# Optimization experiments

Hardware: AMD Instinct MI355X
Metric: run time of the kernel (lower is better)

## Reference

```python
import jax, jax.numpy as jnp
import numpy as np
import itertools
from jax import lax

B, DIM, RES = 32, 256, 8
KEY_DIM, NUM_HEADS, ATTN_RATIO = 16, 8, 4
NH_KD = KEY_DIM * NUM_HEADS          # 128
DH = ATTN_RATIO * KEY_DIM * NUM_HEADS  # 512
HQKV = DH + 2 * NH_KD                # 768
N = RES ** 3                         # 512


def _bias_idxs():
    pts = np.array(list(itertools.product(range(RES), repeat=3)))  # [N,3]
    off = np.abs(pts[:, None, :] - pts[None, :, :])                # [N,N,3]
    return jnp.asarray(off[..., 0] * RES * RES + off[..., 1] * RES + off[..., 2], dtype=jnp.int32)


def setup_inputs() -> dict:
    key = jax.random.key(0)
    ks = jax.random.split(key, 12)
    s = 0.05
    return {
        "x": jax.random.normal(ks[0], (B, DIM, RES, RES, RES), jnp.float32),
        "qkv_w": jax.random.normal(ks[1], (HQKV, DIM), jnp.float32) * s,
        "qkv_scale": jax.random.uniform(ks[2], (HQKV,), jnp.float32, 0.5, 1.5),
        "qkv_bias": jax.random.normal(ks[3], (HQKV,), jnp.float32) * s,
        "dw_w": jax.random.normal(ks[4], (NH_KD, 1, 3, 3, 3), jnp.float32) * s,
        "dw_scale": jax.random.uniform(ks[5], (NH_KD,), jnp.float32, 0.5, 1.5),
        "dw_bias": jax.random.normal(ks[6], (NH_KD,), jnp.float32) * s,
        "attn_biases": jax.random.normal(ks[7], (NUM_HEADS, N), jnp.float32) * s,
        "proj_w": jax.random.normal(ks[8], (DIM, DH), jnp.float32) * s,
        "proj_scale": jax.random.uniform(ks[9], (DIM,), jnp.float32, 0.5, 1.5),
        "proj_bias": jax.random.normal(ks[10], (DIM,), jnp.float32) * s,
        "bias_idxs": _bias_idxs(),
    }


def _cbn(x, w, scale, bias):
    # 1x1x1 Conv3d (pointwise, no bias) + folded BatchNorm (per-channel affine)
    y = jnp.einsum('bcdhw,oc->bodhw', x, w)
    return y * scale[None, :, None, None, None] + bias[None, :, None, None, None]


def reference(x, qkv_w, qkv_scale, qkv_bias, dw_w, dw_scale, dw_bias,
              attn_biases, proj_w, proj_scale, proj_bias, bias_idxs):
    Bx, _, D, H, W = x.shape
    n = D * H * W
    scale = KEY_DIM ** -0.5

    qkv = _cbn(x, qkv_w, qkv_scale, qkv_bias)  # [B, 768, D,H,W]
    q = qkv[:, :NH_KD]
    k = qkv[:, NH_KD:2 * NH_KD]
    v = qkv[:, 2 * NH_KD:]

    # depthwise 3x3x3 conv on q + folded BN
    q = lax.conv_general_dilated(q, dw_w, (1, 1, 1), [(1, 1)] * 3,
                                 dimension_numbers=('NCDHW', 'OIDHW', 'NCDHW'),
                                 feature_group_count=NH_KD)
    q = q * dw_scale[None, :, None, None, None] + dw_bias[None, :, None, None, None]

    q = q.reshape(Bx, NUM_HEADS, KEY_DIM, n)
    k = k.reshape(Bx, NUM_HEADS, KEY_DIM, n)
    v = v.reshape(Bx, NUM_HEADS, DH // NUM_HEADS, n)

    attn = jnp.einsum('bhcn,bhcm->bhnm', q, k) * scale
    attn = attn + attn_biases[:, bias_idxs]          # gathered rel-pos bias [h,N,N]
    attn = jax.nn.softmax(attn, axis=-1)

    out = jnp.einsum('bhdm,bhnm->bhdn', v, attn)     # v @ attn^T
    out = out.reshape(Bx, DH, D, H, W)
    out = jax.nn.relu(out)
    return _cbn(out, proj_w, proj_scale, proj_bias)
```

## Files before the change

kernel.cpp:

```cpp
#include <hip/hip_runtime.h>

typedef unsigned int u32;
typedef unsigned short u16;
typedef __attribute__((ext_vector_type(8))) short bf16x8;
typedef __attribute__((ext_vector_type(4))) float f32x4;

constexpr int BATCH = 32;
constexpr int DIM   = 256;
constexpr int NPTS  = 512;
constexpr int NH    = 8;
constexpr int KD    = 16;
constexpr int DHEAD = 64;
constexpr int NH_KD = 128;
constexpr int DH    = 512;

__device__ __forceinline__ float bflo(u32 u){ return __uint_as_float(u << 16); }
__device__ __forceinline__ float bfhi(u32 u){ return __uint_as_float(u & 0xffff0000u); }
__device__ __forceinline__ float bf2f(u16 u){ return __uint_as_float(((u32)u) << 16); }

__device__ __forceinline__ u32 pack2bf(float a, float b){
  u32 r;
  asm("v_cvt_pk_bf16_f32 %0, %1, %2" : "=v"(r) : "v"(a), "v"(b));
  return r;
}
__device__ __forceinline__ u16 f2bf(float f){ return (u16)pack2bf(f, f); }

union B8 { bf16x8 v; uint2 u2[2]; uint4 u4; };

typedef const __attribute__((address_space(1))) unsigned int gu32_t;
typedef __attribute__((address_space(3))) unsigned int su32_t;
__device__ __forceinline__ void gld16(const u16* src, u16* ldsDst){
  __builtin_amdgcn_global_load_lds((gu32_t*)src, (su32_t*)ldsDst, 16, 0, 0);
}

__device__ __forceinline__ void quadtr(float v[4], int lq){
  float t[4], y[4];
  #pragma unroll
  for (int r = 0; r < 4; r++) t[r] = __shfl_xor(v[r], 1, 64);
  #pragma unroll
  for (int r = 0; r < 4; r++) y[r] = ((r & 1) == (lq & 1)) ? v[r] : t[r ^ 1];
  #pragma unroll
  for (int r = 0; r < 4; r++) t[r] = __shfl_xor(y[r], 2, 64);
  #pragma unroll
  for (int r = 0; r < 4; r++) v[r] = ((r & 2) == (lq & 2)) ? y[r] : t[r ^ 2];
}

__global__ __launch_bounds__(256) void k_pre(
    const float* __restrict__ wq, const float* __restrict__ sq,
    const float* __restrict__ wp, const float* __restrict__ sp,
    u32* __restrict__ wqb, u32* __restrict__ pwb,
    const float* __restrict__ x, u16* __restrict__ xbt,
    const float* __restrict__ ab, const int* __restrict__ bidx,
    u32* __restrict__ biasb)
{
  __shared__ u16 T[64*68];
  const int blk = blockIdx.x;
  const int tid = threadIdx.x;

  if (blk < 640){
    int t = blk * 256 + tid;
    if (t < 98304){
      int i = 2*t;
      float s = sq[i >> 8];
      wqb[t] = pack2bf(wq[i]*s, wq[i+1]*s);
    } else {
      int j = t - 98304;
      int i = 2*j;
      float s = sp[i >> 9];
      pwb[j] = pack2bf(wp[i]*s, wp[i+1]*s);
    }
  } else if (blk < 1664){
    const int bk = blk - 640;
    const int b = bk >> 5, ct = (bk >> 3) & 3, nt = bk & 7;
    const int c0 = ct*64, n0 = nt*64;

    const float* xb = x + ((size_t)b*DIM + c0)*NPTS + n0;
    #pragma unroll
    for (int it = 0; it < 4; it++){
      int cc = (tid >> 4) + it*16;
      int nn = (tid & 15) * 4;
      float4 v = *(const float4*)(xb + (size_t)cc*NPTS + nn);
      u32* dst = (u32*)&T[cc*68 + nn];
      dst[0] = pack2bf(v.x, v.y);
      dst[1] = pack2bf(v.z, v.w);
    }
    __syncthreads();
    u16* ob = xbt + ((size_t)b*NPTS + n0)*DIM + c0;
    #pragma unroll
    for (int it = 0; it < 4; it++){
      int nn = (tid >> 4) + it*16;
      int cc = (tid & 15) * 4;
      uint2 w;
      w.x = (u32)T[(cc+0)*68 + nn] | ((u32)T[(cc+1)*68 + nn] << 16);
      w.y = (u32)T[(cc+2)*68 + nn] | ((u32)T[(cc+3)*68 + nn] << 16);
      *(uint2*)(ob + (size_t)nn*DIM + cc) = w;
    }
  } else {
    const float L2E = 1.4426950408889634f;
    const int bk = blk - 1664;
    const int mtg = bk >> 5, ntile = bk & 31;
    const int lane = tid & 63;
    const int h0 = tid >> 6;
    const int qq = lane >> 4;
    const int n = ntile*16 + (lane & 15);
    int idx[4];
    #pragma unroll
    for (int r = 0; r < 4; r++)
      idx[r] = bidx[(size_t)n*NPTS + mtg*16 + qq*4 + r];
    for (int h = h0; h < NH; h += 4){
      float v0 = ab[h*NPTS + idx[0]] * L2E, v1 = ab[h*NPTS + idx[1]] * L2E;
      float v2 = ab[h*NPTS + idx[2]] * L2E, v3 = ab[h*NPTS + idx[3]] * L2E;
      u32* dst = biasb + (((size_t)(h*32 + mtg)*32 + ntile)*64 + lane)*2;
      dst[0] = pack2bf(v0, v1);
      dst[1] = pack2bf(v2, v3);
    }
  }
}

__global__ __launch_bounds__(256) void k_qkv(
    const u16* __restrict__ xbt, const u16* __restrict__ wqb,
    const float* __restrict__ bias,
    u16* __restrict__ qfb, u16* __restrict__ kb, u16* __restrict__ vb)
{
  const int blk = blockIdx.x;
  const int xcd = blk & 7;
  const int idx = blk >> 3;
  const int pair = xcd*16 + idx/6;
  const int Mblk = idx % 6;
  const int Nblk = pair & 3;
  const int b    = pair >> 2;

  const int tid = threadIdx.x, wave = tid >> 6, lane = tid & 63;
  const int wm = wave >> 1, wn = wave & 1;
  const int c = lane & 15, q = lane >> 4;
  const int lq = lane & 3;
  const int Mbase = Mblk*128 + wm*64;
  const int Nbase = Nblk*128 + wn*64;

  f32x4 acc[4][4];
  #pragma unroll
  for (int mt = 0; mt < 4; mt++){
    f32x4 bi;
    #pragma unroll
    for (int r = 0; r < 4; r++) bi[r] = bias[Mbase + mt*16 + q*4 + r];
    #pragma unroll
    for (int nt = 0; nt < 4; nt++) acc[mt][nt] = bi;
  }

  const u16* xrow = xbt + (size_t)b*NPTS*DIM;

  for (int kc8 = 0; kc8 < 8; kc8++){
    const int kc = kc8*32;
    bf16x8 aW[4], bX[4];
    #pragma unroll
    for (int mt = 0; mt < 4; mt++)
      aW[mt] = *(const bf16x8*)(wqb + (size_t)(Mbase + mt*16 + c)*DIM + kc + q*8);
    #pragma unroll
    for (int nt = 0; nt < 4; nt++)
      bX[nt] = *(const bf16x8*)(xrow + (size_t)(Nbase + nt*16 + c)*DIM + kc + q*8);
    #pragma unroll
    for (int mt = 0; mt < 4; mt++)
      #pragma unroll
      for (int nt = 0; nt < 4; nt++)
        acc[mt][nt] = __builtin_amdgcn_mfma_f32_16x16x32_bf16(
            aW[mt], bX[nt], acc[mt][nt], 0, 0, 0);
  }

  #pragma unroll
  for (int mt = 0; mt < 4; mt++){
    const int m0 = wm*64 + mt*16 + q*4;
    #pragma unroll
    for (int nt = 0; nt < 4; nt++){
      if (Mblk == 1){
        const int n = Nbase + nt*16 + c;
        const int hh = wm*4 + mt;
        uint2 w;
        w.x = pack2bf(acc[mt][nt][0], acc[mt][nt][1]);
        w.y = pack2bf(acc[mt][nt][2], acc[mt][nt][3]);
        *(uint2*)(kb + (((size_t)b*NH + hh)*NPTS + n)*16 + q*4) = w;
      } else {
        float v[4];
        #pragma unroll
        for (int r = 0; r < 4; r++) v[r] = acc[mt][nt][r];
        quadtr(v, lq);
        const int nq = Nbase + nt*16 + (c & ~3);
        uint2 w;
        w.x = pack2bf(v[0], v[1]);
        w.y = pack2bf(v[2], v[3]);
        if (Mblk == 0){
          *(uint2*)(qfb + ((size_t)b*NH_KD + m0 + lq)*NPTS + nq) = w;
        } else {
          const int d = (Mblk - 2)*128 + m0 + lq;
          const int pb = (nq & ~31) | (((nq >> 4) & 1) << 2) | (((nq >> 2) & 3) << 3);
          *(uint2*)(vb + ((size_t)b*DH + d)*NPTS + pb) = w;
        }
      }
    }
  }
}

__global__ __launch_bounds__(512) void k_dw(
    const u16* __restrict__ qfb, const float* __restrict__ dww,
    const float* __restrict__ dws, const float* __restrict__ dwb,
    u16* __restrict__ qb)
{
  const int bc = blockIdx.x;
  const int b  = bc >> 7;
  const int ch = bc & 127;
  const int n  = threadIdx.x;
  const int z = n >> 6, y = (n >> 3) & 7, xx = n & 7;
  float wv[27];
  #pragma unroll
  for (int i = 0; i < 27; i++) wv[i] = dww[ch*27 + i];
  const u16* qp = qfb + (size_t)bc * NPTS;
  float acc = 0.f;
  #pragma unroll
  for (int dz = 0; dz < 3; dz++){
    int zz = z + dz - 1; if ((unsigned)zz > 7u) continue;
    #pragma unroll
    for (int dy = 0; dy < 3; dy++){
      int yy = y + dy - 1; if ((unsigned)yy > 7u) continue;
      #pragma unroll
      for (int dx = 0; dx < 3; dx++){
        int xw = xx + dx - 1; if ((unsigned)xw > 7u) continue;
        acc += bf2f(qp[zz*64 + yy*8 + xw]) * wv[dz*9 + dy*3 + dx];
      }
    }
  }
  acc = (acc * dws[ch] + dwb[ch]) * 0.36067376022224085f;
  int hh = ch >> 4, cc = ch & 15;
  qb[(((size_t)b*NH + hh)*NPTS + n)*16 + cc] = f2bf(acc);
}

__global__ __launch_bounds__(256, 4) void k_attn(
    const u16* __restrict__ qb, const u16* __restrict__ kb,
    const u16* __restrict__ vb, const u16* __restrict__ biasb,
    u16* __restrict__ attnout)
{
  __shared__ u16 VS[2][64][40];

  const int hb = blockIdx.x, tg = blockIdx.y;
  const int b = hb >> 3, h = hb & 7;
  const int tid = threadIdx.x;
  const int lane = tid & 63, wave = tid >> 6;
  const int c = lane & 15, q = lane >> 4;
  const int bh = b*NH + h;
  const int nt0 = tg*8 + wave*2;
  const int n0 = nt0*16;

  const int vr = tid >> 2;
  const int vc = (tid & 3) * 8;

  const bf16x8 zfrag = {0,0,0,0,0,0,0,0};
  bf16x8 bQ0 = zfrag, bQ1 = zfrag;
  if (q < 2){
    bQ0 = *(const bf16x8*)(qb + (((size_t)bh*NPTS + n0 + c) << 4) + q*8);
    bQ1 = *(const bf16x8*)(qb + (((size_t)bh*NPTS + n0 + 16 + c) << 4) + q*8);
  }

  const u16* kbh = kb + ((size_t)bh*NPTS)*16;
  const u16* vbh = vb + ((size_t)b*DH + h*DHEAD)*NPTS;
  const u16* bw0 = biasb + (size_t)h*262144 + (size_t)nt0*256 + lane*4;

  f32x4 O0[4] = {{0,0,0,0},{0,0,0,0},{0,0,0,0},{0,0,0,0}};
  f32x4 O1[4] = {{0,0,0,0},{0,0,0,0},{0,0,0,0},{0,0,0,0}};
  float ls0 = 0.f, ls1 = 0.f;

  bf16x8 aK0, aK1;
  uint2 u00, u01, u10, u11;

  auto loadKB = [&](int win, bf16x8& k0, bf16x8& k1,
                    uint2& x00, uint2& x01, uint2& x10, uint2& x11){
    const int mtg = win*2;
    if (q < 2){
      k0 = *(const bf16x8*)(kbh + (((size_t)(mtg*16 + c)) << 4) + q*8);
      k1 = *(const bf16x8*)(kbh + (((size_t)(mtg*16 + 16 + c)) << 4) + q*8);
    } else { k0 = zfrag; k1 = zfrag; }
    x00 = *(const uint2*)(bw0 + (size_t)mtg*8192);
    x01 = *(const uint2*)(bw0 + (size_t)(mtg+1)*8192);
    x10 = *(const uint2*)(bw0 + 256 + (size_t)mtg*8192);
    x11 = *(const uint2*)(bw0 + 256 + (size_t)(mtg+1)*8192);
  };

  {
    bf16x8 sv = *(const bf16x8*)(vbh + (size_t)vr*NPTS + vc);
    *(bf16x8*)&VS[0][vr][vc] = sv;
  }
  loadKB(0, aK0, aK1, u00, u01, u10, u11);
  __syncthreads();

  #pragma unroll 1
  for (int win = 0; win < 16; win++){
    const int wnext = (win < 15) ? win + 1 : 15;
    bf16x8 sv = *(const bf16x8*)(vbh + (size_t)vr*NPTS + wnext*32 + vc);

    bf16x8 nK0, nK1;
    uint2 m00, m01, m10, m11;
    if (win < 15)
      loadKB(win+1, nK0, nK1, m00, m01, m10, m11);

    const int vbuf = win & 1;
    bf16x8 V0 = *(const bf16x8*)&VS[vbuf][ 0 + c][q*8];
    bf16x8 V1 = *(const bf16x8*)&VS[vbuf][16 + c][q*8];
    bf16x8 V2 = *(const bf16x8*)&VS[vbuf][32 + c][q*8];
    bf16x8 V3 = *(const bf16x8*)&VS[vbuf][48 + c][q*8];

    f32x4 c00, c01, c10, c11;
    c00[0]=bflo(u00.x); c00[1]=bfhi(u00.x); c00[2]=bflo(u00.y); c00[3]=bfhi(u00.y);
    c01[0]=bflo(u01.x); c01[1]=bfhi(u01.x); c01[2]=bflo(u01.y); c01[3]=bfhi(u01.y);
    c10[0]=bflo(u10.x); c10[1]=bfhi(u10.x); c10[2]=bflo(u10.y); c10[3]=bfhi(u10.y);
    c11[0]=bflo(u11.x); c11[1]=bfhi(u11.x); c11[2]=bflo(u11.y); c11[3]=bfhi(u11.y);
    f32x4 S00 = __builtin_amdgcn_mfma_f32_16x16x32_bf16(aK0, bQ0, c00, 0, 0, 0);
    f32x4 S01 = __builtin_amdgcn_mfma_f32_16x16x32_bf16(aK1, bQ0, c01, 0, 0, 0);
    f32x4 S10 = __builtin_amdgcn_mfma_f32_16x16x32_bf16(aK0, bQ1, c10, 0, 0, 0);
    f32x4 S11 = __builtin_amdgcn_mfma_f32_16x16x32_bf16(aK1, bQ1, c11, 0, 0, 0);

    float e0, e1, e2, e3;
    B8 aP0, aP1;
    e0 = __builtin_amdgcn_exp2f(S00[0]); e1 = __builtin_amdgcn_exp2f(S00[1]);
    e2 = __builtin_amdgcn_exp2f(S00[2]); e3 = __builtin_amdgcn_exp2f(S00[3]);
    ls0 += (e0 + e1) + (e2 + e3);
    aP0.u4.x = pack2bf(e0, e1); aP0.u4.y = pack2bf(e2, e3);
    e0 = __builtin_amdgcn_exp2f(S01[0]); e1 = __builtin_amdgcn_exp2f(S01[1]);
    e2 = __builtin_amdgcn_exp2f(S01[2]); e3 = __builtin_amdgcn_exp2f(S01[3]);
    ls0 += (e0 + e1) + (e2 + e3);
    aP0.u4.z = pack2bf(e0, e1); aP0.u4.w = pack2bf(e2, e3);
    e0 = __builtin_amdgcn_exp2f(S10[0]); e1 = __builtin_amdgcn_exp2f(S10[1]);
    e2 = __builtin_amdgcn_exp2f(S10[2]); e3 = __builtin_amdgcn_exp2f(S10[3]);
    ls1 += (e0 + e1) + (e2 + e3);
    aP1.u4.x = pack2bf(e0, e1); aP1.u4.y = pack2bf(e2, e3);
    e0 = __builtin_amdgcn_exp2f(S11[0]); e1 = __builtin_amdgcn_exp2f(S11[1]);
    e2 = __builtin_amdgcn_exp2f(S11[2]); e3 = __builtin_amdgcn_exp2f(S11[3]);
    ls1 += (e0 + e1) + (e2 + e3);
    aP1.u4.z = pack2bf(e0, e1); aP1.u4.w = pack2bf(e2, e3);

    O0[0] = __builtin_amdgcn_mfma_f32_16x16x32_bf16(aP0.v, V0, O0[0], 0, 0, 0);
    O1[0] = __builtin_amdgcn_mfma_f32_16x16x32_bf16(aP1.v, V0, O1[0], 0, 0, 0);
    O0[1] = __builtin_amdgcn_mfma_f32_16x16x32_bf16(aP0.v, V1, O0[1], 0, 0, 0);
    O1[1] = __builtin_amdgcn_mfma_f32_16x16x32_bf16(aP1.v, V1, O1[1], 0, 0, 0);
    O0[2] = __builtin_amdgcn_mfma_f32_16x16x32_bf16(aP0.v, V2, O0[2], 0, 0, 0);
    O1[2] = __builtin_amdgcn_mfma_f32_16x16x32_bf16(aP1.v, V2, O1[2], 0, 0, 0);
    O0[3] = __builtin_amdgcn_mfma_f32_16x16x32_bf16(aP0.v, V3, O0[3], 0, 0, 0);
    O1[3] = __builtin_amdgcn_mfma_f32_16x16x32_bf16(aP1.v, V3, O1[3], 0, 0, 0);

    if (win < 15)
      *(bf16x8*)&VS[wnext & 1][vr][vc] = sv;
    __syncthreads();

    aK0 = nK0; aK1 = nK1;
    u00 = m00; u01 = m01; u10 = m10; u11 = m11;
  }

  ls0 += __shfl_xor(ls0, 16, 64);
  ls0 += __shfl_xor(ls0, 32, 64);
  ls1 += __shfl_xor(ls1, 16, 64);
  ls1 += __shfl_xor(ls1, 32, 64);
  f32x4 inv0, inv1;
  #pragma unroll
  for (int r = 0; r < 4; r++){
    inv0[r] = 1.0f / __shfl(ls0, q*4 + r, 64);
    inv1[r] = 1.0f / __shfl(ls1, q*4 + r, 64);
  }

  u16* ao = attnout + ((size_t)(b*NPTS + n0))*DH + h*DHEAD;
  #pragma unroll
  for (int dt = 0; dt < 4; dt++)
    #pragma unroll
    for (int r = 0; r < 4; r++){
      ao[(size_t)(q*4 + r)*DH + dt*16 + c] =
          f2bf(fmaxf(O0[dt][r]*inv0[r], 0.f));
      ao[(size_t)(16 + q*4 + r)*DH + dt*16 + c] =
          f2bf(fmaxf(O1[dt][r]*inv1[r], 0.f));
    }
}

__global__ __launch_bounds__(256) void k_proj(
    const u16* __restrict__ attn, const u16* __restrict__ pwb,
    const float* __restrict__ bias, float* __restrict__ out)
{
  __shared__ u16 As[2][4096];
  __shared__ u16 Bs[2][2048];

  const int blk = blockIdx.x;
  const int xcd = blk & 7;
  const int idx = blk >> 3;
  const int b    = xcd*4 + (idx >> 4);
  const int inner = idx & 15;
  const int Nblk = inner >> 1;
  const int Mblk = inner & 1;

  const int tid = threadIdx.x, wave = tid >> 6, lane = tid & 63;
  const int wm = wave >> 1, wn = wave & 1;
  const int c = lane & 15, q = lane >> 4;
  const int Mbase = Mblk*128 + wm*64;
  const int Nbase = Nblk*64 + wn*32;

  f32x4 acc[4][2];
  #pragma unroll
  for (int mt = 0; mt < 4; mt++){
    f32x4 bi;
    #pragma unroll
    for (int r = 0; r < 4; r++) bi[r] = bias[Mbase + mt*16 + q*4 + r];
    #pragma unroll
    for (int nt = 0; nt < 2; nt++) acc[mt][nt] = bi;
  }

  const u16* aT = pwb + (size_t)(Mblk*128)*DH;
  const u16* bT = attn + ((size_t)b*NPTS + Nblk*64)*DH;

  const int srow = lane >> 2, scol = (lane & 3)*8;

  auto STAGE = [&](int buf, int kc){
    #pragma unroll
    for (int i = 0; i < 2; i++){
      const int ch = wave*2 + i;
      gld16(aT + (size_t)(ch*16 + srow)*DH + kc + scol, &As[buf][ch*512]);
    }
    gld16(bT + (size_t)(wave*16 + srow)*DH + kc + scol, &Bs[buf][wave*512]);
  };

  STAGE(0, 0);
  __syncthreads();

  int cur = 0;
  #pragma unroll 2
  for (int ks = 0; ks < 16; ks++){
    if (ks < 15) STAGE(cur^1, (ks+1)*32);
    bf16x8 aW[4], bA[2];
    #pragma unroll
    for (int mt = 0; mt < 4; mt++)
      aW[mt] = *(const bf16x8*)&As[cur][(wm*64 + mt*16 + c)*32 + q*8];
    #pragma unroll
    for (int nt = 0; nt < 2; nt++)
      bA[nt] = *(const bf16x8*)&Bs[cur][(wn*32 + nt*16 + c)*32 + q*8];
    #pragma unroll
    for (int mt = 0; mt < 4; mt++)
      #pragma unroll
      for (int nt = 0; nt < 2; nt++)
        acc[mt][nt] = __builtin_amdgcn_mfma_f32_16x16x32_bf16(
            aW[mt], bA[nt], acc[mt][nt], 0, 0, 0);
    __syncthreads();
    cur ^= 1;
  }

  #pragma unroll
  for (int mt = 0; mt < 4; mt++){
    #pragma unroll
    for (int nt = 0; nt < 2; nt++){
      const int n = Nbase + nt*16 + c;
      #pragma unroll
      for (int r = 0; r < 4; r++){
        int o = Mbase + mt*16 + q*4 + r;
        out[((size_t)b*DIM + o)*NPTS + n] = acc[mt][nt][r];
      }
    }
  }
}

extern "C" void kernel_launch(void* const* d_in, const int* in_sizes, int n_in,
                              void* d_out, int out_size, void* d_ws, size_t ws_size,
                              hipStream_t stream)
{
  const float* x     = (const float*)d_in[0];
  const float* qkv_w = (const float*)d_in[1];
  const float* qkv_s = (const float*)d_in[2];
  const float* qkv_b = (const float*)d_in[3];
  const float* dw_w  = (const float*)d_in[4];
  const float* dw_s  = (const float*)d_in[5];
  const float* dw_b  = (const float*)d_in[6];
  const float* ab    = (const float*)d_in[7];
  const float* pw    = (const float*)d_in[8];
  const float* ps    = (const float*)d_in[9];
  const float* pb    = (const float*)d_in[10];
  const int* bidx    = (const int*)d_in[11];

  char* ws = (char*)d_ws;
  u16*   qfb   = (u16*)  (ws);
  u16*   qb    = (u16*)  (ws + ( 4u << 20));
  u16*   kb    = (u16*)  (ws + ( 8u << 20));
  u16*   vb    = (u16*)  (ws + (12u << 20));
  u16*   attn  = (u16*)  (ws + (28u << 20));
  u32*   biasb = (u32*)  (ws + (44u << 20));
  u32*   wqb   = (u32*)  (ws + (48u << 20));
  u32*   pwb   = (u32*)  (ws + (49u << 20));
  u16*   xbt   = (u16*)  (ws + (50u << 20));

  k_pre <<<dim3(2688),     256, 0, stream>>>(qkv_w, qkv_s, pw, ps, wqb, pwb,
                                             x, xbt, ab, bidx, biasb);
  k_qkv <<<dim3(768),      256, 0, stream>>>(xbt, (const u16*)wqb, qkv_b, qfb, kb, vb);
  k_dw  <<<dim3(32*128),   512, 0, stream>>>(qfb, dw_w, dw_s, dw_b, qb);
  k_attn<<<dim3(256, 4),   256, 0, stream>>>(qb, kb, vb, (const u16*)biasb, attn);
  k_proj<<<dim3(512),      256, 0, stream>>>(attn, (const u16*)pwb, pb, (float*)d_out);
}
```

Measured before the change: 182.4 us.

## Fuse depthwise 3x3x3 conv into attention kernel prologue

Removes the separate depthwise-conv kernel and computes each attention block's 128 query rows directly from the pre-conv q buffer in the attention kernel's prologue. Each thread computes an 8-wide x row using vectorized row loads and writes the result to a new shared-memory Q tile, which waves read after the existing barrier. This saves one launch and the round trip of the q intermediate through global memory. In exchange, halo rows are recomputed redundantly across blocks, and the prologue adds register pressure and latency before the main loop.

```diff
diff --git a/kernel.cpp b/kernel.cpp
--- a/kernel.cpp
+++ b/kernel.cpp
@@ -199,45 +199,15 @@
   }
 }
 
-__global__ __launch_bounds__(512) void k_dw(
-    const u16* __restrict__ qfb, const float* __restrict__ dww,
-    const float* __restrict__ dws, const float* __restrict__ dwb,
-    u16* __restrict__ qb)
-{
-  const int bc = blockIdx.x;
-  const int b  = bc >> 7;
-  const int ch = bc & 127;
-  const int n  = threadIdx.x;
-  const int z = n >> 6, y = (n >> 3) & 7, xx = n & 7;
-  float wv[27];
-  #pragma unroll
-  for (int i = 0; i < 27; i++) wv[i] = dww[ch*27 + i];
-  const u16* qp = qfb + (size_t)bc * NPTS;
-  float acc = 0.f;
-  #pragma unroll
-  for (int dz = 0; dz < 3; dz++){
-    int zz = z + dz - 1; if ((unsigned)zz > 7u) continue;
-    #pragma unroll
-    for (int dy = 0; dy < 3; dy++){
-      int yy = y + dy - 1; if ((unsigned)yy > 7u) continue;
-      #pragma unroll
-      for (int dx = 0; dx < 3; dx++){
-        int xw = xx + dx - 1; if ((unsigned)xw > 7u) continue;
-        acc += bf2f(qp[zz*64 + yy*8 + xw]) * wv[dz*9 + dy*3 + dx];
-      }
-    }
-  }
-  acc = (acc * dws[ch] + dwb[ch]) * 0.36067376022224085f;
-  int hh = ch >> 4, cc = ch & 15;
-  qb[(((size_t)b*NH + hh)*NPTS + n)*16 + cc] = f2bf(acc);
-}
-
 __global__ __launch_bounds__(256, 4) void k_attn(
-    const u16* __restrict__ qb, const u16* __restrict__ kb,
+    const u16* __restrict__ qfb, const u16* __restrict__ kb,
     const u16* __restrict__ vb, const u16* __restrict__ biasb,
+    const float* __restrict__ dww, const float* __restrict__ dws,
+    const float* __restrict__ dwb,
     u16* __restrict__ attnout)
 {
   __shared__ u16 VS[2][64][40];
+  __shared__ u16 QS[128][16];
 
   const int hb = blockIdx.x, tg = blockIdx.y;
   const int b = hb >> 3, h = hb & 7;
@@ -251,21 +221,60 @@
   const int vr = tid >> 2;
   const int vc = (tid & 3) * 8;
 
-  const bf16x8 zfrag = {0,0,0,0,0,0,0,0};
-  bf16x8 bQ0 = zfrag, bQ1 = zfrag;
-  if (q < 2){
-    bQ0 = *(const bf16x8*)(qb + (((size_t)bh*NPTS + n0 + c) << 4) + q*8);
-    bQ1 = *(const bf16x8*)(qb + (((size_t)bh*NPTS + n0 + 16 + c) << 4) + q*8);
-  }
-
   const u16* kbh = kb + ((size_t)bh*NPTS)*16;
   const u16* vbh = vb + ((size_t)b*DH + h*DHEAD)*NPTS;
   const u16* bw0 = biasb + (size_t)h*262144 + (size_t)nt0*256 + lane*4;
 
-  f32x4 O0[4] = {{0,0,0,0},{0,0,0,0},{0,0,0,0},{0,0,0,0}};
-  f32x4 O1[4] = {{0,0,0,0},{0,0,0,0},{0,0,0,0},{0,0,0,0}};
-  float ls0 = 0.f, ls1 = 0.f;
-
+  bf16x8 sv0 = *(const bf16x8*)(vbh + (size_t)vr*NPTS + vc);
+
+  {
+    const int row = tid >> 4;
+    const int rz  = row >> 3, ry = row & 7;
+    const int chl = tid & 15;
+    const int qch = h*16 + chl;
+    const int z0  = tg*2;
+
+    float wv[27];
+    #pragma unroll
+    for (int i = 0; i < 27; i++) wv[i] = dww[qch*27 + i];
+    const float sc = dws[qch], bi = dwb[qch];
+    const u16* qrow = qfb + ((size_t)b*NH_KD + qch)*NPTS;
+
+    float acc8[8];
+    #pragma unroll
+    for (int xo = 0; xo < 8; xo++) acc8[xo] = 0.f;
+
+    #pragma unroll
+    for (int dz = 0; dz < 3; dz++){
+      int zz = z0 + rz + dz - 1; if ((unsigned)zz > 7u) continue;
+      #pragma unroll
+      for (int dy = 0; dy < 3; dy++){
+        int yy = ry + dy - 1; if ((unsigned)yy > 7u) continue;
+        B8 rvb; rvb.v = *(const bf16x8*)(qrow + zz*64 + yy*8);
+        float r[8];
+        #pragma unroll
+        for (int xo = 0; xo < 8; xo++) r[xo] = bf2f(((const u16*)&rvb)[xo]);
+        #pragma unroll
+        for (int dx = 0; dx < 3; dx++){
+          float w = wv[dz*9 + dy*3 + dx];
+          #pragma unroll
+          for (int xo = 0; xo < 8; xo++){
+            int xx = xo + dx - 1;
+            if (xx >= 0 && xx < 8) acc8[xo] += r[xx]*w;
+          }
+        }
+      }
+    }
+    #pragma unroll
+    for (int xo = 0; xo < 8; xo++){
+      float v = (acc8[xo]*sc + bi) * 0.36067376022224085f;
+      QS[row*8 + xo][chl] = f2bf(v);
+    }
+  }
+
+  *(bf16x8*)&VS[0][vr][vc] = sv0;
+
+  const bf16x8 zfrag = {0,0,0,0,0,0,0,0};
   bf16x8 aK0, aK1;
   uint2 u00, u01, u10, u11;
 
@@ -282,12 +291,18 @@
     x11 = *(const uint2*)(bw0 + 256 + (size_t)(mtg+1)*8192);
   };
 
-  {
-    bf16x8 sv = *(const bf16x8*)(vbh + (size_t)vr*NPTS + vc);
-    *(bf16x8*)&VS[0][vr][vc] = sv;
-  }
   loadKB(0, aK0, aK1, u00, u01, u10, u11);
   __syncthreads();
+
+  bf16x8 bQ0 = zfrag, bQ1 = zfrag;
+  if (q < 2){
+    bQ0 = *(const bf16x8*)&QS[wave*32 + c][q*8];
+    bQ1 = *(const bf16x8*)&QS[wave*32 + 16 + c][q*8];
+  }
+
+  f32x4 O0[4] = {{0,0,0,0},{0,0,0,0},{0,0,0,0},{0,0,0,0}};
+  f32x4 O1[4] = {{0,0,0,0},{0,0,0,0},{0,0,0,0},{0,0,0,0}};
+  float ls0 = 0.f, ls1 = 0.f;
 
   #pragma unroll 1
   for (int win = 0; win < 16; win++){
@@ -476,7 +491,6 @@
 
   char* ws = (char*)d_ws;
   u16*   qfb   = (u16*)  (ws);
-  u16*   qb    = (u16*)  (ws + ( 4u << 20));
   u16*   kb    = (u16*)  (ws + ( 8u << 20));
   u16*   vb    = (u16*)  (ws + (12u << 20));
   u16*   attn  = (u16*)  (ws + (28u << 20));
@@ -488,7 +502,7 @@
   k_pre <<<dim3(2688),     256, 0, stream>>>(qkv_w, qkv_s, pw, ps, wqb, pwb,
                                              x, xbt, ab, bidx, biasb);
   k_qkv <<<dim3(768),      256, 0, stream>>>(xbt, (const u16*)wqb, qkv_b, qfb, kb, vb);
-  k_dw  <<<dim3(32*128),   512, 0, stream>>>(qfb, dw_w, dw_s, dw_b, qb);
-  k_attn<<<dim3(256, 4),   256, 0, stream>>>(qb, kb, vb, (const u16*)biasb, attn);
+  k_attn<<<dim3(256, 4),   256, 0, stream>>>(qfb, kb, vb, (const u16*)biasb,
+                                             dw_w, dw_s, dw_b, attn);
   k_proj<<<dim3(512),      256, 0, stream>>>(attn, (const u16*)pwb, pb, (float*)d_out);
 }
```

Result: faster. 160.3 us (-12.1%).
